# Kernel optimization log

Hardware: AMD Instinct MI355X
Metric: run time of the kernel (lower is better)

Reference implementation:

```python
import jax, jax.numpy as jnp
import numpy as np


def _sobel_filters():
    # fil is the 3x3 smoothing kernel [[1,2,1],[2,4,2],[1,2,1]]
    fil = np.array([[1, 2, 1], [2, 4, 2], [1, 2, 1]], dtype=np.float32)
    fx = np.zeros((3, 3, 3), dtype=np.float32)
    fx[0, :, :] = fil
    fx[2, :, :] = -fil
    fy = np.zeros((3, 3, 3), dtype=np.float32)
    fy[:, 0, :] = fil
    fy[:, 2, :] = -fil
    fz = np.zeros((3, 3, 3), dtype=np.float32)
    fz[:, :, 0] = fil
    fz[:, :, 2] = -fil
    # Stack the three fixed (non-learned) filters as 3 output channels: [O=3, I=1, 3,3,3]
    return jnp.asarray(np.stack([fx, fy, fz])[:, None])


_FILT = _sobel_filters()
_DN = ('NCDHW', 'OIDHW', 'NCDHW')


def _grad3d(v):
    # v: [N,1,D,H,W] -> [N,3,D,H,W], padding=1 == SAME for 3x3x3 stride 1
    return jax.lax.conv_general_dilated(
        v, _FILT.astype(v.dtype), window_strides=(1, 1, 1),
        padding='SAME', dimension_numbers=_DN)


def setup_inputs() -> dict:
    key = jax.random.key(0)
    k1, k2 = jax.random.split(key)
    shape = (2, 1, 160, 192, 224)
    x = jax.random.normal(k1, shape, dtype=jnp.float32)
    y = jax.random.normal(k2, shape, dtype=jnp.float32)
    return {"x": x, "y": y}


def reference(x, y):
    gx = _grad3d(x)  # [N,3,D,H,W]
    gy = _grad3d(y)
    d2 = (gx - gy) ** 2
    # sum over the 3 directions of the per-direction MSE
    return jnp.sum(jnp.mean(d2, axis=(0, 2, 3, 4)))
```

## Files before the change

### kernel.cpp

```cpp
#include <hip/hip_runtime.h>
#include <stdint.h>


#define N_  2
#define D_  160
#define H_  192
#define W_  224
#define PS  (H_ * W_)

#define TD  8
#define TH  8
constexpr int SROWS = TH + 2;
constexpr int RPAD  = 256;
constexpr float SCALE = 1.0f / ((float)N_ * D_ * H_ * W_);

#define DMA16(gp, lp) __builtin_amdgcn_global_load_lds(                        \
    (const __attribute__((address_space(1))) void*)(gp),                       \
    (__attribute__((address_space(3))) void*)(lp), 16, 0, 0)

__global__ __launch_bounds__(256, 2)
void grad_loss_kernel(const float* __restrict__ x, const float* __restrict__ y,
                      float* __restrict__ out) {
    __shared__ float sbuf[3][SROWS][2][RPAD];
    __shared__ float wsum[4];

    const int tid  = threadIdx.x;
    const int lane = tid & 63;
    const int wv   = tid >> 6;

    const int h0 = blockIdx.y * TH;
    const int nchunks = D_ / TD;
    const int nb = blockIdx.z / nchunks;
    const int d0 = (blockIdx.z % nchunks) * TD;

    const float* vbx = x + (size_t)nb * ((size_t)D_ * PS);
    const float* vby = y + (size_t)nb * ((size_t)D_ * PS);

    const int lo = (lane < 56 ? lane : 55) * 4;

    int sl[5], sa[5], srw[5];
    const float* sb[5];
    #pragma unroll
    for (int k = 0; k < 5; ++k) {
        int item = 5 * wv + k;
        sl[k] = item >> 1;
        sa[k] = item & 1;
        int gh  = h0 - 1 + sl[k];
        int ghc = min(max(gh, 0), H_ - 1);
        srw[k] = ghc * W_;
        sb[k]  = sa[k] ? vby : vbx;
    }

    auto stage = [&](int p, int bsel) {
        int pc = min(max(p, 0), D_ - 1);
        size_t poff = (size_t)pc * PS;
        #pragma unroll
        for (int k = 0; k < 5; ++k)
            DMA16(sb[k] + poff + srw[k] + lo, &sbuf[bsel][sl[k]][sa[k]][0]);
    };

    const bool wact = lane < 56;
    float rmask[4];
    #pragma unroll
    for (int r = 0; r < 4; ++r) {
        int gh = h0 - 1 + 2 * wv + r;
        rmask[r] = (((unsigned)gh < (unsigned)H_) && wact) ? 1.f : 0.f;
    }
    const int lrd = lane * 4;

    float4 A0[2], A1[2], A2[2], B0[2], B1[2], B2[2];
    const float4 z4 = make_float4(0.f, 0.f, 0.f, 0.f);
    #pragma unroll
    for (int j = 0; j < 2; ++j) { A0[j]=A1[j]=A2[j]=B0[j]=B1[j]=B2[j]=z4; }
    float acc = 0.f;

    stage(d0 - 1, 0);
    asm volatile("" ::: "memory");
    stage(d0, 1);

    #pragma unroll
    for (int it = 0; it < TD + 2; ++it) {
        if (it == TD + 1)
            asm volatile("s_waitcnt vmcnt(0)\n\ts_barrier" ::: "memory");
        else
            asm volatile("s_waitcnt vmcnt(5)\n\ts_barrier" ::: "memory");

        if (it <= TD - 1) stage(d0 + 1 + it, (it + 2) % 3);

        const int q = d0 - 1 + it;
        const float pm = (q >= 0 && q < D_) ? 1.f : 0.f;
        const int bsel = it % 3;

        float4 sw[4], gw[4];
        #pragma unroll
        for (int r = 0; r < 4; ++r) {
            const int l = 2 * wv + r;
            const float4 xr = *(const float4*)&sbuf[bsel][l][0][lrd];
            const float4 yr = *(const float4*)&sbuf[bsel][l][1][lrd];
            const float m = rmask[r] * pm;
            float4 v = make_float4((xr.x - yr.x) * m, (xr.y - yr.y) * m,
                                   (xr.z - yr.z) * m, (xr.w - yr.w) * m);
            float Lm = __shfl_up(v.w, 1, 64);
            float Rp = __shfl_down(v.x, 1, 64);
            if (lane == 0) Lm = 0.f;
            sw[r] = make_float4(Lm + 2.f * v.x + v.y,
                                v.x + 2.f * v.y + v.z,
                                v.y + 2.f * v.z + v.w,
                                v.z + 2.f * v.w + Rp);
            gw[r] = make_float4(Lm - v.y, v.x - v.z, v.y - v.w, v.z - Rp);
        }
        float4 n0[2], n1[2], n2[2];
        #pragma unroll
        for (int j = 0; j < 2; ++j) {
            n0[j] = make_float4(sw[j].x + 2.f * sw[j+1].x + sw[j+2].x,
                                sw[j].y + 2.f * sw[j+1].y + sw[j+2].y,
                                sw[j].z + 2.f * sw[j+1].z + sw[j+2].z,
                                sw[j].w + 2.f * sw[j+1].w + sw[j+2].w);
            n1[j] = make_float4(sw[j].x - sw[j+2].x, sw[j].y - sw[j+2].y,
                                sw[j].z - sw[j+2].z, sw[j].w - sw[j+2].w);
            n2[j] = make_float4(gw[j].x + 2.f * gw[j+1].x + gw[j+2].x,
                                gw[j].y + 2.f * gw[j+1].y + gw[j+2].y,
                                gw[j].z + 2.f * gw[j+1].z + gw[j+2].z,
                                gw[j].w + 2.f * gw[j+1].w + gw[j+2].w);
        }

        if (it >= 2 && wact) {
            #pragma unroll
            for (int j = 0; j < 2; ++j) {
                float4 gx = make_float4(A0[j].x - n0[j].x, A0[j].y - n0[j].y,
                                        A0[j].z - n0[j].z, A0[j].w - n0[j].w);
                float4 gy = make_float4(A1[j].x + 2.f * B1[j].x + n1[j].x,
                                        A1[j].y + 2.f * B1[j].y + n1[j].y,
                                        A1[j].z + 2.f * B1[j].z + n1[j].z,
                                        A1[j].w + 2.f * B1[j].w + n1[j].w);
                float4 gz = make_float4(A2[j].x + 2.f * B2[j].x + n2[j].x,
                                        A2[j].y + 2.f * B2[j].y + n2[j].y,
                                        A2[j].z + 2.f * B2[j].z + n2[j].z,
                                        A2[j].w + 2.f * B2[j].w + n2[j].w);
                acc = fmaf(gx.x, gx.x, acc); acc = fmaf(gx.y, gx.y, acc);
                acc = fmaf(gx.z, gx.z, acc); acc = fmaf(gx.w, gx.w, acc);
                acc = fmaf(gy.x, gy.x, acc); acc = fmaf(gy.y, gy.y, acc);
                acc = fmaf(gy.z, gy.z, acc); acc = fmaf(gy.w, gy.w, acc);
                acc = fmaf(gz.x, gz.x, acc); acc = fmaf(gz.y, gz.y, acc);
                acc = fmaf(gz.z, gz.z, acc); acc = fmaf(gz.w, gz.w, acc);
            }
        }

        #pragma unroll
        for (int j = 0; j < 2; ++j) {
            A0[j] = B0[j]; A1[j] = B1[j]; A2[j] = B2[j];
            B0[j] = n0[j]; B1[j] = n1[j]; B2[j] = n2[j];
        }
    }

    #pragma unroll
    for (int off = 32; off > 0; off >>= 1)
        acc += __shfl_xor(acc, off, 64);
    if (lane == 0) wsum[wv] = acc;
    __syncthreads();
    if (tid == 0) {
        float s = (wsum[0] + wsum[1]) + (wsum[2] + wsum[3]);
        atomicAdd(out, s * SCALE);
    }
}

extern "C" void kernel_launch(void* const* d_in, const int* in_sizes, int n_in,
                              void* d_out, int out_size, void* d_ws, size_t ws_size,
                              hipStream_t stream) {
    const float* x = (const float*)d_in[0];
    const float* y = (const float*)d_in[1];
    float* out = (float*)d_out;

    hipMemsetAsync(out, 0, sizeof(float), stream);

    dim3 block(256);
    dim3 grid(1,
              H_ / TH,
              N_ * (D_ / TD));
    grad_loss_kernel<<<grid, block, 0, stream>>>(x, y, out);
}
```

Measured before the change: 138.1 us.

## Use single-wave blocks with barrier-free 4-deep LDS DMA pipeline

Each block shrinks to one 64-lane wave that handles two output rows, loading all four halo rows itself into a 4-slot LDS ring. Because one wave owns its buffer, s_barrier disappears and only vmcnt waits remain, and prefetch depth grows from two to three planes. The cost is redundant halo loads (4 input rows per 2 output rows instead of 10 per 8), roughly 1.6x more global/L2 traffic, plus four times as many blocks and atomics.

```diff
diff --git a/kernel.cpp b/kernel.cpp
--- a/kernel.cpp
+++ b/kernel.cpp
@@ -8,27 +8,23 @@
 #define W_  224
 #define PS  (H_ * W_)
 
-#define TD  8
-#define TH  8
-constexpr int SROWS = TH + 2;
-constexpr int RPAD  = 256;
+#define TD   8
+#define NBUF 4
+constexpr int RPAD = 256;
 constexpr float SCALE = 1.0f / ((float)N_ * D_ * H_ * W_);
 
 #define DMA16(gp, lp) __builtin_amdgcn_global_load_lds(                        \
     (const __attribute__((address_space(1))) void*)(gp),                       \
     (__attribute__((address_space(3))) void*)(lp), 16, 0, 0)
 
-__global__ __launch_bounds__(256, 2)
+__global__ __launch_bounds__(64, 1)
 void grad_loss_kernel(const float* __restrict__ x, const float* __restrict__ y,
                       float* __restrict__ out) {
-    __shared__ float sbuf[3][SROWS][2][RPAD];
-    __shared__ float wsum[4];
+    __shared__ float sbuf[NBUF][4][2][RPAD];
 
-    const int tid  = threadIdx.x;
-    const int lane = tid & 63;
-    const int wv   = tid >> 6;
+    const int lane = threadIdx.x;
 
-    const int h0 = blockIdx.y * TH;
+    const int h0 = blockIdx.y * 2;
     const int nchunks = D_ / TD;
     const int nb = blockIdx.z / nchunks;
     const int d0 = (blockIdx.z % nchunks) * TD;
@@ -38,34 +34,27 @@
 
     const int lo = (lane < 56 ? lane : 55) * 4;
 
-    int sl[5], sa[5], srw[5];
-    const float* sb[5];
+    const float* sp[8];
     #pragma unroll
-    for (int k = 0; k < 5; ++k) {
-        int item = 5 * wv + k;
-        sl[k] = item >> 1;
-        sa[k] = item & 1;
-        int gh  = h0 - 1 + sl[k];
-        int ghc = min(max(gh, 0), H_ - 1);
-        srw[k] = ghc * W_;
-        sb[k]  = sa[k] ? vby : vbx;
+    for (int k = 0; k < 4; ++k) {
+        int ghc = min(max(h0 - 1 + k, 0), H_ - 1);
+        sp[2 * k + 0] = vbx + ghc * W_ + lo;
+        sp[2 * k + 1] = vby + ghc * W_ + lo;
     }
 
     auto stage = [&](int p, int bsel) {
         int pc = min(max(p, 0), D_ - 1);
         size_t poff = (size_t)pc * PS;
         #pragma unroll
-        for (int k = 0; k < 5; ++k)
-            DMA16(sb[k] + poff + srw[k] + lo, &sbuf[bsel][sl[k]][sa[k]][0]);
+        for (int i = 0; i < 8; ++i)
+            DMA16(sp[i] + poff, &sbuf[bsel][i >> 1][i & 1][0]);
     };
 
     const bool wact = lane < 56;
     float rmask[4];
     #pragma unroll
-    for (int r = 0; r < 4; ++r) {
-        int gh = h0 - 1 + 2 * wv + r;
-        rmask[r] = (((unsigned)gh < (unsigned)H_) && wact) ? 1.f : 0.f;
-    }
+    for (int r = 0; r < 4; ++r)
+        rmask[r] = (((unsigned)(h0 - 1 + r) < (unsigned)H_) && wact) ? 1.f : 0.f;
     const int lrd = lane * 4;
 
     float4 A0[2], A1[2], A2[2], B0[2], B1[2], B2[2];
@@ -75,28 +64,24 @@
     float acc = 0.f;
 
     stage(d0 - 1, 0);
-    asm volatile("" ::: "memory");
-    stage(d0, 1);
+    stage(d0,     1);
+    stage(d0 + 1, 2);
 
     #pragma unroll
     for (int it = 0; it < TD + 2; ++it) {
-        if (it == TD + 1)
-            asm volatile("s_waitcnt vmcnt(0)\n\ts_barrier" ::: "memory");
-        else
-            asm volatile("s_waitcnt vmcnt(5)\n\ts_barrier" ::: "memory");
+        asm volatile("s_waitcnt vmcnt(16)" ::: "memory");
 
-        if (it <= TD - 1) stage(d0 + 1 + it, (it + 2) % 3);
+        stage(d0 + 2 + it, (it + 3) % NBUF);
 
         const int q = d0 - 1 + it;
         const float pm = (q >= 0 && q < D_) ? 1.f : 0.f;
-        const int bsel = it % 3;
+        const int bsel = it % NBUF;
 
         float4 sw[4], gw[4];
         #pragma unroll
         for (int r = 0; r < 4; ++r) {
-            const int l = 2 * wv + r;
-            const float4 xr = *(const float4*)&sbuf[bsel][l][0][lrd];
-            const float4 yr = *(const float4*)&sbuf[bsel][l][1][lrd];
+            const float4 xr = *(const float4*)&sbuf[bsel][r][0][lrd];
+            const float4 yr = *(const float4*)&sbuf[bsel][r][1][lrd];
             const float m = rmask[r] * pm;
             float4 v = make_float4((xr.x - yr.x) * m, (xr.y - yr.y) * m,
                                    (xr.z - yr.z) * m, (xr.w - yr.w) * m);
@@ -153,15 +138,12 @@
         }
     }
 
+    asm volatile("s_waitcnt vmcnt(0)" ::: "memory");
+
     #pragma unroll
     for (int off = 32; off > 0; off >>= 1)
         acc += __shfl_xor(acc, off, 64);
-    if (lane == 0) wsum[wv] = acc;
-    __syncthreads();
-    if (tid == 0) {
-        float s = (wsum[0] + wsum[1]) + (wsum[2] + wsum[3]);
-        atomicAdd(out, s * SCALE);
-    }
+    if (lane == 0) atomicAdd(out, acc * SCALE);
 }
 
 extern "C" void kernel_launch(void* const* d_in, const int* in_sizes, int n_in,
@@ -173,9 +155,9 @@
 
     hipMemsetAsync(out, 0, sizeof(float), stream);
 
-    dim3 block(256);
+    dim3 block(64);
     dim3 grid(1,
-              H_ / TH,
+              H_ / 2,
               N_ * (D_ / TD));
     grad_loss_kernel<<<grid, block, 0, stream>>>(x, y, out);
 }
```

Result: slower. 181.1 us (+31.1%).
